# Kernel optimization log

Hardware: AMD Instinct MI355X
Metric: run time of the kernel (lower is better)

## Reference

```python
import jax, jax.numpy as jnp
import numpy as np

ALPHA = 32.0 ** 2
HEADS = 8
DIM_HEAD = 64
EPS = 1e-5


def _leaky(x):
    return jnp.where(x >= 0, x, 0.1 * x)


def _cpb_bias(fmap_size, w0, b0, w1, b1, w2, b2):
    # continuous position bias: MLP over signed-log relative coords -> [h, n, n]
    pos = jnp.arange(fmap_size)
    gi, gj = jnp.meshgrid(pos, pos, indexing='ij')
    grid = jnp.stack([gi, gj], axis=-1).reshape(-1, 2)  # [n, 2]
    rel = grid[:, None, :] - grid[None, :, :]           # [n, n, 2]
    rel = jnp.sign(rel) * jnp.log(jnp.abs(rel) + 1.0)
    h = _leaky(jnp.einsum('ijc,dc->ijd', rel.astype(jnp.float32), w0) + b0)
    h = _leaky(jnp.einsum('ijc,dc->ijd', h, w1) + b1)
    h = jnp.einsum('ijc,hc->ijh', h, w2) + b2           # [n, n, heads]
    return jnp.transpose(h, (2, 0, 1))                  # [heads, n, n]


def _stable_softmax(t, alpha=ALPHA):
    t = t / alpha
    t = t - jax.lax.stop_gradient(jnp.max(t, axis=-1, keepdims=True))
    return jax.nn.softmax(t * alpha, axis=-1)


def setup_inputs() -> dict:
    key = jax.random.key(0)
    ks = jax.random.split(key, 9)
    B, C, H, W = 8, 512, 32, 32
    inner = HEADS * DIM_HEAD
    s = 0.05
    return {
        'x': jax.random.normal(ks[0], (B, C, H, W), jnp.float32),
        'gamma': jnp.ones((1, C, 1, 1), jnp.float32),
        'w_qkv': jax.random.normal(ks[1], (inner * 3, C), jnp.float32) * s,
        'w_out': jax.random.normal(ks[2], (C, inner), jnp.float32) * s,
        'cpb_w0': jax.random.normal(ks[3], (128, 2), jnp.float32) * s,
        'cpb_b0': jax.random.normal(ks[4], (128,), jnp.float32) * s,
        'cpb_w1': jax.random.normal(ks[5], (128, 128), jnp.float32) * s,
        'cpb_b1': jax.random.normal(ks[6], (128,), jnp.float32) * s,
        'cpb_w2': jax.random.normal(ks[7], (HEADS, 128), jnp.float32) * s,
        'cpb_b2': jax.random.normal(ks[8], (HEADS,), jnp.float32) * s,
    }


def reference(x, gamma, w_qkv, w_out, cpb_w0, cpb_b0, cpb_w1, cpb_b1, cpb_w2, cpb_b2):
    B, C, H, W = x.shape
    n = H * W
    scale = DIM_HEAD ** -0.5
    residual = x

    # LayerNormChan: normalize over channel dim with biased variance
    mean = jnp.mean(x, axis=1, keepdims=True)
    var = jnp.var(x, axis=1, keepdims=True)
    xn = (x - mean) / jnp.sqrt(var + EPS) * gamma

    # 1x1 conv qkv projection as matmul over channels
    xf = xn.reshape(B, C, n)                              # [B, C, n]
    qkv = jnp.einsum('oc,bcn->bon', w_qkv, xf)            # [B, 3*inner, n]
    q, k, v = jnp.split(qkv, 3, axis=1)
    rs = lambda t: t.reshape(B, HEADS, DIM_HEAD, n)
    q, k, v = rs(q), rs(k), rs(v)

    sim = jnp.einsum('bhdi,bhdj->bhij', q, k) * scale     # [B, h, n, n]
    bias = _cpb_bias(H, cpb_w0, cpb_b0, cpb_w1, cpb_b1, cpb_w2, cpb_b2)
    sim = sim + bias[None]

    attn = _stable_softmax(sim)
    out = jnp.einsum('bhij,bhdj->bhdi', attn, v)          # [B, h, d, n]
    out = out.reshape(B, HEADS * DIM_HEAD, n)
    out = jnp.einsum('oc,bcn->bon', w_out, out).reshape(B, C, H, W)
    return out + residual
```

## Files before the change

### kernel.cpp

```cpp
#include <hip/hip_runtime.h>
#include <hip/hip_bf16.h>

#define CCH   512
#define BATCH 8
#define NPOS  1024
#define MQKV  1536
#define EPS   1e-5f
#define LOG2E 1.4426950408889634f

typedef __attribute__((ext_vector_type(4))) float f32x4;
typedef __attribute__((ext_vector_type(8))) __bf16 bf16x8;
typedef __attribute__((ext_vector_type(8))) unsigned short u16x8;
typedef __attribute__((ext_vector_type(4))) unsigned short u16x4;

__device__ inline unsigned short f2bf(float f) {
  __hip_bfloat16 h = __float2bfloat16(f);
  return __builtin_bit_cast(unsigned short, h);
}
__device__ inline float bf2f(unsigned short u) {
  return __bfloat162float(__builtin_bit_cast(__hip_bfloat16, u));
}

__device__ inline int sw(int row, int col) { return row * 64 + (col ^ ((row & 7) << 3)); }
__device__ inline int swk(int row, int col) { return row * 64 + (col ^ (((row >> 2) & 7) << 3)); }
__device__ inline int sw32(int row, int lh) {
  return row * 32 + ((lh ^ ((row ^ (row >> 2)) & 3)) << 3);
}

__device__ inline void gload16(const void* g, void* l) {
  __builtin_amdgcn_global_load_lds((const __attribute__((address_space(1))) void*)g,
                                   (__attribute__((address_space(3))) void*)l, 16, 0, 0);
}

#define CBAR(N) do {                                              \
    asm volatile("s_waitcnt vmcnt(" #N ")" ::: "memory");         \
    asm volatile("s_waitcnt lgkmcnt(0)" ::: "memory");            \
    __builtin_amdgcn_s_barrier();                                 \
  } while (0)

__global__ __launch_bounds__(256) void setup_kernel(
    const float* __restrict__ wq, const float* __restrict__ wo,
    unsigned short* __restrict__ wqb, unsigned short* __restrict__ wob,
    const float* __restrict__ x, const float* __restrict__ gamma,
    unsigned short* __restrict__ xnT,
    const float* __restrict__ table, unsigned short* __restrict__ biasP) {
  __shared__ float red[4][32][2];
  __shared__ float gsh[512];
  __shared__ unsigned short obuf[32 * 520];
  int bid = blockIdx.x, tid = threadIdx.x;

  if (bid >= 3328) {
    int base = ((bid - 3328) * 256 + tid) * 8;
    int h = base >> 20;
    int i = (base >> 10) & 1023;
    int j0 = base & 1023;
    int ib = i >> 5, il = i & 31;
    u16x8 outv;
    #pragma unroll
    for (int e = 0; e < 8; ++e) {
      int j = j0 + e;
      int dy = ib - (j >> 5) + 31;
      int dx = il - (j & 31) + 31;
      outv[e] = f2bf(table[h * 3969 + dy * 63 + dx]);
    }
    *(u16x8*)&biasP[base] = outv;
    return;
  }

  if (bid < 3072) {
    int i = bid * 256 + tid;
    if (i < MQKV * CCH) {
      float v = wq[i];
      if (i < 512 * CCH) v *= 0.125f * LOG2E;
      wqb[i] = f2bf(v);
    }
    if (i < CCH * CCH) wob[i] = f2bf(wo[i]);
  } else {
    int blk = bid - 3072;
    int b = blk >> 5, p0 = (blk & 31) * 32;
    int pl = tid & 31, wv = tid >> 6, cg = tid >> 5;
    gsh[tid] = gamma[tid];
    gsh[tid + 256] = gamma[tid + 256];
    const float* xp = x + (size_t)b * CCH * NPOS + p0 + pl;
    float vals[64];
    float s1 = 0.f, s2 = 0.f;
    #pragma unroll
    for (int j = 0; j < 64; ++j) {
      float v = xp[(size_t)(cg + 8 * j) * NPOS];
      vals[j] = v; s1 += v; s2 += v * v;
    }
    s1 += __shfl_xor(s1, 32, 64); s2 += __shfl_xor(s2, 32, 64);
    if ((tid & 63) < 32) { red[wv][pl][0] = s1; red[wv][pl][1] = s2; }
    __syncthreads();
    float t1 = 0.f, t2 = 0.f;
    #pragma unroll
    for (int w2i = 0; w2i < 4; ++w2i) { t1 += red[w2i][pl][0]; t2 += red[w2i][pl][1]; }
    float mean = t1 * (1.f / 512.f);
    float var = t2 * (1.f / 512.f) - mean * mean;
    float rstd = rsqrtf(var + EPS);
    #pragma unroll
    for (int j = 0; j < 64; ++j) {
      int c = cg + 8 * j;
      obuf[pl * 520 + c] = f2bf((vals[j] - mean) * rstd * gsh[c]);
    }
    __syncthreads();
    unsigned short* orow = xnT + ((size_t)b * NPOS + p0) * 512;
    #pragma unroll
    for (int i = 0; i < 8; ++i) {
      int c2 = tid + i * 256;
      int pp = c2 >> 6, ch = c2 & 63;
      *(u16x8*)&orow[(size_t)pp * 512 + ch * 8] = *(const u16x8*)&obuf[pp * 520 + ch * 8];
    }
  }
}

__global__ __launch_bounds__(256) void cpb_kernel(
    const float* __restrict__ w0, const float* __restrict__ b0,
    const float* __restrict__ w1, const float* __restrict__ b1,
    const float* __restrict__ w2, const float* __restrict__ b2,
    float* __restrict__ table) {
  __shared__ float w1s[128 * 129];
  __shared__ float w2s[8 * 128];
  __shared__ float sh1[2][128];
  __shared__ float sh2[2][128];
  int tid = threadIdx.x;
  #pragma unroll
  for (int i = 0; i < 64; ++i) {
    int idx = i * 256 + tid;
    w1s[(idx >> 7) * 129 + (idx & 127)] = w1[idx];
  }
  #pragma unroll
  for (int i = 0; i < 4; ++i) {
    int idx = i * 256 + tid;
    w2s[idx] = w2[idx];
  }
  int sub = tid >> 7, t = tid & 127;
  float w00 = w0[t * 2 + 0], w01 = w0[t * 2 + 1], bb0 = b0[t], bb1 = b1[t];
  int hh = t >> 4, k16 = t & 15;
  float b2h = b2[hh];
  __syncthreads();

  #pragma unroll 1
  for (int pass = 0; pass < 8; ++pass) {
    int d0 = (blockIdx.x * 8 + pass) * 2 + sub;
    bool ok = d0 < 3969;
    int d0c = ok ? d0 : 0;
    int dy = d0c / 63 - 31, dx = d0c % 63 - 31;
    float r0 = (dy > 0 ? 1.f : (dy < 0 ? -1.f : 0.f)) * logf(fabsf((float)dy) + 1.f);
    float r1 = (dx > 0 ? 1.f : (dx < 0 ? -1.f : 0.f)) * logf(fabsf((float)dx) + 1.f);
    float h0 = r0 * w00 + r1 * w01 + bb0;
    sh1[sub][t] = (h0 >= 0.f) ? h0 : 0.1f * h0;
    __syncthreads();
    float a = bb1;
    #pragma unroll 8
    for (int c = 0; c < 128; ++c) a += sh1[sub][c] * w1s[t * 129 + c];
    sh2[sub][t] = (a >= 0.f) ? a : 0.1f * a;
    __syncthreads();
    float o = 0.f;
    #pragma unroll
    for (int c = 0; c < 8; ++c) o += sh2[sub][k16 * 8 + c] * w2s[hh * 128 + k16 * 8 + c];
    #pragma unroll
    for (int mm = 1; mm < 16; mm <<= 1) o += __shfl_xor(o, mm, 64);
    if (k16 == 0 && ok) table[hh * 3969 + d0] = (o + b2h) * LOG2E;
    __syncthreads();
  }
}

__global__ __launch_bounds__(256) void gemm_qkv(const unsigned short* __restrict__ Ag,
                                                const unsigned short* __restrict__ Bg,
                                                unsigned short* __restrict__ qT,
                                                unsigned short* __restrict__ kT,
                                                unsigned short* __restrict__ vB) {
  __shared__ unsigned short smem[24576];
  int tid = threadIdx.x;
  int by = blockIdx.y;
  int m0 = by * 128, nn0 = blockIdx.x * 128;
  int wave = tid >> 6, lane = tid & 63;
  int wm = wave >> 1, wn = wave & 1;
  int l16 = lane & 15, lh = lane >> 4;
  int r4 = lane >> 2, c4 = lane & 3;
  int csw = ((c4 ^ (r4 & 3) ^ ((lane >> 4) & 3))) << 3;
  f32x4 acc[4][4];
  #pragma unroll
  for (int it = 0; it < 4; ++it)
    #pragma unroll
    for (int jt = 0; jt < 4; ++jt) acc[it][jt] = (f32x4){0.f, 0.f, 0.f, 0.f};

  #define GSTAGE(bsel, k0) do {                                                               \
    _Pragma("unroll")                                                                         \
    for (int i_ = 0; i_ < 2; ++i_) {                                                          \
      int grp_ = wave * 2 + i_;                                                               \
      int row_ = grp_ * 16 + r4;                                                              \
      gload16(&Ag[(size_t)(m0 + row_) * 512 + (k0) + csw], smem + (bsel) * 4096 + grp_ * 512);\
      gload16(&Bg[(size_t)(nn0 + row_) * 512 + (k0) + csw],                                   \
              smem + 12288 + (bsel) * 4096 + grp_ * 512);                                     \
    }                                                                                         \
  } while (0)

  GSTAGE(0, 0);
  GSTAGE(1, 32);
  asm volatile("s_waitcnt vmcnt(4)" ::: "memory");
  __builtin_amdgcn_s_barrier();
  int cur = 0;
  #pragma unroll 1
  for (int k = 0; k < 16; ++k) {
    int stg = (cur == 0) ? 2 : cur - 1;
    if (k < 14) GSTAGE(stg, (k + 2) * 32);
    const unsigned short* As = smem + cur * 4096;
    const unsigned short* Bs = smem + 12288 + cur * 4096;
    bf16x8 a[4], b[4];
    #pragma unroll
    for (int it = 0; it < 4; ++it) a[it] = *(const bf16x8*)&As[sw32(wm * 64 + it * 16 + l16, lh)];
    #pragma unroll
    for (int jt = 0; jt < 4; ++jt) b[jt] = *(const bf16x8*)&Bs[sw32(wn * 64 + jt * 16 + l16, lh)];
    __builtin_amdgcn_s_setprio(1);
    #pragma unroll
    for (int it = 0; it < 4; ++it)
      #pragma unroll
      for (int jt = 0; jt < 4; ++jt)
        acc[it][jt] = __builtin_amdgcn_mfma_f32_16x16x32_bf16(a[it], b[jt], acc[it][jt], 0, 0, 0);
    __builtin_amdgcn_s_setprio(0);
    if (k < 14) CBAR(4); else CBAR(0);
    cur = (cur == 2) ? 0 : cur + 1;
  }

  int sel = by >> 2;
  int hh0 = (by & 3) * 2;
  int bb = nn0 >> 10, p0 = nn0 & 1023;
  unsigned short* Cs = smem;
  if (sel < 2) {
    #pragma unroll
    for (int it = 0; it < 4; ++it)
      #pragma unroll
      for (int jt = 0; jt < 4; ++jt) {
        int nnl = wn * 64 + jt * 16 + l16;
        int mb = wm * 64 + it * 16 + lh * 4;
        #pragma unroll
        for (int r = 0; r < 4; ++r)
          Cs[nnl * 128 + ((mb + r) ^ ((nnl & 7) << 4))] = f2bf(acc[it][jt][r]);
      }
    __syncthreads();
    unsigned short* dst = (sel == 0) ? qT : kT;
    #pragma unroll
    for (int i = 0; i < 8; ++i) {
      int c = tid + i * 256;
      int hl = c >> 10, p = (c >> 3) & 127, ch = c & 7;
      int mb = hl * 64 + ch * 8;
      u16x8 val = *(u16x8*)&Cs[p * 128 + (mb ^ ((p & 7) << 4))];
      int bh = bb * 8 + hh0 + hl;
      *(u16x8*)&dst[((size_t)bh * 1024 + p0 + p) * 64 + ch * 8] = val;
    }
  } else {
    #pragma unroll
    for (int it = 0; it < 4; ++it)
      #pragma unroll
      for (int jt = 0; jt < 4; ++jt) {
        int nnl = wn * 64 + jt * 16 + l16;
        int mb = wm * 64 + it * 16 + lh * 4;
        #pragma unroll
        for (int r = 0; r < 4; ++r)
          Cs[(mb + r) * 128 + (nnl ^ (((mb + r) & 7) << 4))] = f2bf(acc[it][jt][r]);
      }
    __syncthreads();
    #pragma unroll
    for (int i = 0; i < 8; ++i) {
      int c = tid + i * 256;
      int mloc = c >> 4, ch = c & 15;
      u16x8 val = *(u16x8*)&Cs[mloc * 128 + ((ch * 8) ^ ((mloc & 7) << 4))];
      int d = mloc & 63, hl = mloc >> 6;
      int bh = bb * 8 + hh0 + hl;
      *(u16x8*)&vB[((size_t)bh * 64 + d) * 1024 + p0 + ch * 8] = val;
    }
  }
}

__global__ __launch_bounds__(256) void gemm_out(const unsigned short* __restrict__ Ag,
                                                const unsigned short* __restrict__ Bg,
                                                const float* __restrict__ xres,
                                                float* __restrict__ yout) {
  __shared__ unsigned short smem[18432];
  int tid = threadIdx.x;
  int m0 = blockIdx.y * 64, nn0 = blockIdx.x * 128;
  int wave = tid >> 6, lane = tid & 63;
  int wm = wave >> 1, wn = wave & 1;
  int l16 = lane & 15, lh = lane >> 4;
  int r4 = lane >> 2, c4 = lane & 3;
  int csw = ((c4 ^ (r4 & 3) ^ ((lane >> 4) & 3))) << 3;
  f32x4 acc[2][4];
  #pragma unroll
  for (int it = 0; it < 2; ++it)
    #pragma unroll
    for (int jt = 0; jt < 4; ++jt) acc[it][jt] = (f32x4){0.f, 0.f, 0.f, 0.f};

  #define OSTAGE(bsel, k0) do {                                                               \
    {                                                                                         \
      int row_ = wave * 16 + r4;                                                              \
      gload16(&Ag[(size_t)(m0 + row_) * 512 + (k0) + csw],                                    \
              smem + (bsel) * 2048 + wave * 512);                                             \
    }                                                                                         \
    _Pragma("unroll")                                                                         \
    for (int i_ = 0; i_ < 2; ++i_) {                                                          \
      int grp_ = wave * 2 + i_;                                                               \
      int row_ = grp_ * 16 + r4;                                                              \
      gload16(&Bg[(size_t)(nn0 + row_) * 512 + (k0) + csw],                                   \
              smem + 6144 + (bsel) * 4096 + grp_ * 512);                                      \
    }                                                                                         \
  } while (0)

  OSTAGE(0, 0);
  OSTAGE(1, 32);
  asm volatile("s_waitcnt vmcnt(3)" ::: "memory");
  __builtin_amdgcn_s_barrier();
  int cur = 0;
  #pragma unroll 1
  for (int k = 0; k < 16; ++k) {
    int stg = (cur == 0) ? 2 : cur - 1;
    if (k < 14) OSTAGE(stg, (k + 2) * 32);
    const unsigned short* As = smem + cur * 2048;
    const unsigned short* Bs = smem + 6144 + cur * 4096;
    bf16x8 a[2], b[4];
    #pragma unroll
    for (int it = 0; it < 2; ++it) a[it] = *(const bf16x8*)&As[sw32(wm * 32 + it * 16 + l16, lh)];
    #pragma unroll
    for (int jt = 0; jt < 4; ++jt) b[jt] = *(const bf16x8*)&Bs[sw32(wn * 64 + jt * 16 + l16, lh)];
    __builtin_amdgcn_s_setprio(1);
    #pragma unroll
    for (int it = 0; it < 2; ++it)
      #pragma unroll
      for (int jt = 0; jt < 4; ++jt)
        acc[it][jt] = __builtin_amdgcn_mfma_f32_16x16x32_bf16(a[it], b[jt], acc[it][jt], 0, 0, 0);
    __builtin_amdgcn_s_setprio(0);
    if (k < 14) CBAR(3); else CBAR(0);
    cur = (cur == 2) ? 0 : cur + 1;
  }

  #pragma unroll
  for (int it = 0; it < 2; ++it) {
    int mbase = m0 + wm * 32 + it * 16 + lh * 4;
    #pragma unroll
    for (int jt = 0; jt < 4; ++jt) {
      int nn = nn0 + wn * 64 + jt * 16 + l16;
      int bb = nn >> 10, p = nn & 1023;
      #pragma unroll
      for (int r = 0; r < 4; ++r) {
        size_t addr = ((size_t)bb * 512 + mbase + r) * 1024 + p;
        yout[addr] = acc[it][jt][r] + xres[addr];
      }
    }
  }
}

__global__ __launch_bounds__(512) void attn_kernel(const unsigned short* __restrict__ qT,
                                                   const unsigned short* __restrict__ kT,
                                                   const unsigned short* __restrict__ vB,
                                                   const unsigned short* __restrict__ biasP,
                                                   unsigned short* __restrict__ attnout) {
  __shared__ unsigned short Kbuf[3][64 * 64];
  __shared__ unsigned short Vbuf[3][64 * 64];
  __shared__ unsigned short Ps[8][16 * 64];
  int tid = threadIdx.x;
  int bh = blockIdx.x;
  int i0 = blockIdx.y * 128;
  int hh = bh & 7, bb = bh >> 3;
  int w = tid >> 6, lane = tid & 63, l16 = lane & 15, lh = lane >> 4;
  int rsub = lane >> 3, csub = lane & 7;
  int scswV = (csub ^ rsub) * 8;
  int scswK = (csub ^ ((w * 2 + (rsub >> 2)) & 7)) * 8;

  const unsigned short* kbase = kT + (size_t)bh * NPOS * 64;
  const unsigned short* vbase = vB + (size_t)bh * 64 * NPOS;
  const unsigned short* bptr  = biasP + ((size_t)hh * 1024 + i0 + w * 16) * 1024 + l16 * 4;

  int qrow = i0 + w * 16 + l16;
  const unsigned short* qb = qT + ((size_t)bh * NPOS + qrow) * 64 + lh * 8;
  bf16x8 qreg[2];
  qreg[0] = *(const bf16x8*)&qb[0];
  qreg[1] = *(const bf16x8*)&qb[32];

  f32x4 o[5];
  #pragma unroll
  for (int dt = 0; dt < 5; ++dt) o[dt] = (f32x4){0.f, 0.f, 0.f, 0.f};

  bf16x8 ones;
  {
    u16x8 tmp = {0x3F80, 0x3F80, 0x3F80, 0x3F80, 0x3F80, 0x3F80, 0x3F80, 0x3F80};
    ones = __builtin_bit_cast(bf16x8, tmp);
  }

  #define STAGE(Kd, Vd, jj) do {                                                        \
    gload16(&kbase[(size_t)((jj) + w * 8 + rsub) * 64 + scswK], &(Kd)[w * 512]);        \
    gload16(&vbase[(size_t)(w * 8 + rsub) * 1024 + (jj) + scswV], &(Vd)[w * 512]);      \
  } while (0)

  STAGE(Kbuf[0], Vbuf[0], 0);
  STAGE(Kbuf[1], Vbuf[1], 64);
  asm volatile("s_waitcnt vmcnt(2)" ::: "memory");
  __builtin_amdgcn_s_barrier();
  int cur = 0;

  #pragma unroll 1
  for (int t = 0; t < 16; ++t) {
    int j0 = t * 64;

    u16x4 bv4[4];
    #pragma unroll
    for (int r = 0; r < 4; ++r) bv4[r] = *(const u16x4*)&bptr[(lh * 4 + r) * 1024 + j0];

    int stg = (cur == 0) ? 2 : cur - 1;
    if (t < 14) STAGE(Kbuf[stg], Vbuf[stg], j0 + 128);

    const unsigned short* Ks = Kbuf[cur];
    const unsigned short* Vs = Vbuf[cur];

    f32x4 s[4];
    #pragma unroll
    for (int jt = 0; jt < 4; ++jt) s[jt] = (f32x4){0.f, 0.f, 0.f, 0.f};
    __builtin_amdgcn_s_setprio(1);
    #pragma unroll
    for (int ks = 0; ks < 2; ++ks) {
      int koff = ks * 32 + lh * 8;
      #pragma unroll
      for (int jt = 0; jt < 4; ++jt) {
        bf16x8 bk = *(const bf16x8*)&Ks[swk(l16 * 4 + jt, koff)];
        s[jt] = __builtin_amdgcn_mfma_f32_16x16x32_bf16(qreg[ks], bk, s[jt], 0, 0, 0);
      }
    }
    __builtin_amdgcn_s_setprio(0);

    #pragma unroll
    for (int r = 0; r < 4; ++r) {
      int rloc = lh * 4 + r;
      u16x4 pq;
      #pragma unroll
      for (int jt = 0; jt < 4; ++jt)
        pq[jt] = f2bf(__builtin_amdgcn_exp2f(s[jt][r] + bf2f(bv4[r][jt])));
      *(u16x4*)&Ps[w][sw(rloc, l16 * 4)] = pq;
    }

    __builtin_amdgcn_s_setprio(1);
    #pragma unroll
    for (int js = 0; js < 2; ++js) {
      int koff = js * 32 + lh * 8;
      bf16x8 pa = *(const bf16x8*)&Ps[w][sw(l16, koff)];
      #pragma unroll
      for (int dt = 0; dt < 4; ++dt) {
        bf16x8 vb = *(const bf16x8*)&Vs[sw(dt * 16 + l16, koff)];
        o[dt] = __builtin_amdgcn_mfma_f32_16x16x32_bf16(pa, vb, o[dt], 0, 0, 0);
      }
      o[4] = __builtin_amdgcn_mfma_f32_16x16x32_bf16(pa, ones, o[4], 0, 0, 0);
    }
    __builtin_amdgcn_s_setprio(0);

    if (t < 14) CBAR(2); else CBAR(0);
    cur = (cur == 2) ? 0 : cur + 1;
  }

  #pragma unroll
  for (int r = 0; r < 4; ++r) {
    float inv = 1.f / o[4][r];
    int gi = i0 + w * 16 + lh * 4 + r;
    #pragma unroll
    for (int dt = 0; dt < 4; ++dt)
      attnout[((size_t)bb * 1024 + gi) * 512 + hh * 64 + dt * 16 + l16] = f2bf(o[dt][r] * inv);
  }
}

extern "C" void kernel_launch(void* const* d_in, const int* in_sizes, int n_in,
                              void* d_out, int out_size, void* d_ws, size_t ws_size,
                              hipStream_t stream) {
  const float* x     = (const float*)d_in[0];
  const float* gamma = (const float*)d_in[1];
  const float* w_qkv = (const float*)d_in[2];
  const float* w_out = (const float*)d_in[3];
  const float* cw0   = (const float*)d_in[4];
  const float* cb0   = (const float*)d_in[5];
  const float* cw1   = (const float*)d_in[6];
  const float* cb1   = (const float*)d_in[7];
  const float* cw2   = (const float*)d_in[8];
  const float* cb2   = (const float*)d_in[9];
  float* out = (float*)d_out;

  char* ws = (char*)d_ws;
  unsigned short* xnT   = (unsigned short*)(ws + 0);
  unsigned short* wqb   = (unsigned short*)(ws + 8388608);
  unsigned short* wob   = (unsigned short*)(ws + 9961472);
  unsigned short* qT    = (unsigned short*)(ws + 10485760);
  unsigned short* kT    = (unsigned short*)(ws + 18874368);
  unsigned short* vB    = (unsigned short*)(ws + 27262976);
  float*          table = (float*)(ws + 35651584);
  unsigned short* biasP = (unsigned short*)(ws + 35782656);
  unsigned short* aout  = (unsigned short*)(ws + 52559872);

  cpb_kernel<<<256, 256, 0, stream>>>(cw0, cb0, cw1, cb1, cw2, cb2, table);
  setup_kernel<<<7424, 256, 0, stream>>>(w_qkv, w_out, wqb, wob, x, gamma, xnT, table, biasP);
  gemm_qkv<<<dim3(64, 12), 256, 0, stream>>>(wqb, xnT, qT, kT, vB);
  attn_kernel<<<dim3(64, 8), 512, 0, stream>>>(qT, kT, vB, biasP, aout);
  gemm_out<<<dim3(64, 8), 256, 0, stream>>>(wob, aout, x, out);
}
```

Before: 100.7 us.

## Vectorize weight conversion and prefetch attention bias one tile ahead

New measurement: 99.39 us (median of 2 runs). No clear change (-1.3%).

```diff
diff --git a/kernel.cpp b/kernel.cpp
--- a/kernel.cpp
+++ b/kernel.cpp
@@ -49,8 +49,8 @@
   __shared__ unsigned short obuf[32 * 520];
   int bid = blockIdx.x, tid = threadIdx.x;
 
-  if (bid >= 3328) {
-    int base = ((bid - 3328) * 256 + tid) * 8;
+  if (bid >= 640) {
+    int base = ((bid - 640) * 256 + tid) * 8;
     int h = base >> 20;
     int i = (base >> 10) & 1023;
     int j0 = base & 1023;
@@ -67,16 +67,29 @@
     return;
   }
 
-  if (bid < 3072) {
-    int i = bid * 256 + tid;
-    if (i < MQKV * CCH) {
-      float v = wq[i];
-      if (i < 512 * CCH) v *= 0.125f * LOG2E;
-      wqb[i] = f2bf(v);
-    }
-    if (i < CCH * CCH) wob[i] = f2bf(wo[i]);
+  if (bid < 384) {
+    int base = bid * 2048 + tid * 8;
+    float sc = (base < 512 * CCH) ? (0.125f * LOG2E) : 1.0f;
+    f32x4 v0 = *(const f32x4*)&wq[base];
+    f32x4 v1 = *(const f32x4*)&wq[base + 4];
+    u16x8 outv;
+    #pragma unroll
+    for (int e = 0; e < 4; ++e) outv[e] = f2bf(v0[e] * sc);
+    #pragma unroll
+    for (int e = 0; e < 4; ++e) outv[4 + e] = f2bf(v1[e] * sc);
+    *(u16x8*)&wqb[base] = outv;
+    if (base < CCH * CCH) {
+      f32x4 w0v = *(const f32x4*)&wo[base];
+      f32x4 w1v = *(const f32x4*)&wo[base + 4];
+      u16x8 ov;
+      #pragma unroll
+      for (int e = 0; e < 4; ++e) ov[e] = f2bf(w0v[e]);
+      #pragma unroll
+      for (int e = 0; e < 4; ++e) ov[4 + e] = f2bf(w1v[e]);
+      *(u16x8*)&wob[base] = ov;
+    }
   } else {
-    int blk = bid - 3072;
+    int blk = bid - 384;
     int b = blk >> 5, p0 = (blk & 31) * 32;
     int pl = tid & 31, wv = tid >> 6, cg = tid >> 5;
     gsh[tid] = gamma[tid];
@@ -393,8 +406,11 @@
   } while (0)
 
   STAGE(Kbuf[0], Vbuf[0], 0);
+  u16x4 bvc[4];
+  #pragma unroll
+  for (int r = 0; r < 4; ++r) bvc[r] = *(const u16x4*)&bptr[(lh * 4 + r) * 1024];
   STAGE(Kbuf[1], Vbuf[1], 64);
-  asm volatile("s_waitcnt vmcnt(2)" ::: "memory");
+  asm volatile("s_waitcnt vmcnt(6)" ::: "memory");
   __builtin_amdgcn_s_barrier();
   int cur = 0;
 
@@ -402,9 +418,11 @@
   for (int t = 0; t < 16; ++t) {
     int j0 = t * 64;
 
-    u16x4 bv4[4];
-    #pragma unroll
-    for (int r = 0; r < 4; ++r) bv4[r] = *(const u16x4*)&bptr[(lh * 4 + r) * 1024 + j0];
+    u16x4 bvn[4];
+    if (t < 15) {
+      #pragma unroll
+      for (int r = 0; r < 4; ++r) bvn[r] = *(const u16x4*)&bptr[(lh * 4 + r) * 1024 + j0 + 64];
+    }
 
     int stg = (cur == 0) ? 2 : cur - 1;
     if (t < 14) STAGE(Kbuf[stg], Vbuf[stg], j0 + 128);
@@ -433,7 +451,7 @@
       u16x4 pq;
       #pragma unroll
       for (int jt = 0; jt < 4; ++jt)
-        pq[jt] = f2bf(__builtin_amdgcn_exp2f(s[jt][r] + bf2f(bv4[r][jt])));
+        pq[jt] = f2bf(__builtin_amdgcn_exp2f(s[jt][r] + bf2f(bvc[r][jt])));
       *(u16x4*)&Ps[w][sw(rloc, l16 * 4)] = pq;
     }
 
@@ -451,7 +469,14 @@
     }
     __builtin_amdgcn_s_setprio(0);
 
-    if (t < 14) CBAR(2); else CBAR(0);
+    if (t < 15) {
+      #pragma unroll
+      for (int r = 0; r < 4; ++r) bvc[r] = bvn[r];
+    }
+
+    if (t < 14) CBAR(6);
+    else if (t == 14) CBAR(4);
+    else CBAR(0);
     cur = (cur == 2) ? 0 : cur + 1;
   }
 
@@ -492,7 +517,7 @@
   unsigned short* aout  = (unsigned short*)(ws + 52559872);
 
   cpb_kernel<<<256, 256, 0, stream>>>(cw0, cb0, cw1, cb1, cw2, cb2, table);
-  setup_kernel<<<7424, 256, 0, stream>>>(w_qkv, w_out, wqb, wob, x, gamma, xnT, table, biasP);
+  setup_kernel<<<4736, 256, 0, stream>>>(w_qkv, w_out, wqb, wob, x, gamma, xnT, table, biasP);
   gemm_qkv<<<dim3(64, 12), 256, 0, stream>>>(wqb, xnT, qT, kT, vB);
   attn_kernel<<<dim3(64, 8), 512, 0, stream>>>(qT, kT, vB, biasP, aout);
   gemm_out<<<dim3(64, 8), 256, 0, stream>>>(wob, aout, x, out);
```
